# Optimization experiments

Measured on AMD Instinct MI355X. Metric: run time of the kernel, lower is better.

## Reference

```python
import jax, jax.numpy as jnp
import numpy as np

T, B, E, H = 2048, 4, 1024, 16
D = E // H  # head_dim = 64


def setup_inputs() -> dict:
    key = jax.random.key(0)
    k1, k2, k3, k4 = jax.random.split(key, 4)
    x = jax.random.normal(k1, (T, B, E), dtype=jnp.float32)
    # xavier-ish init scale
    Wqkv = jax.random.normal(k2, (3 * E, E), dtype=jnp.float32) * (1.0 / np.sqrt(2.0 * E))
    Wo = jax.random.normal(k3, (E, E), dtype=jnp.float32) * (1.0 / np.sqrt(E))
    key_padding_mask = jax.random.randint(k4, (B, T), 0, 2).astype(jnp.bool_)  # True = pad
    return {"x": x, "Wqkv": Wqkv, "Wo": Wo, "key_padding_mask": key_padding_mask}


def reference(x, Wqkv, Wo, key_padding_mask):
    t, b, e = x.shape
    h, d = H, E // H
    # fused QKV projection (bias=False)
    qkv = jnp.einsum('tbe,fe->tbf', x, Wqkv).reshape(t, b, 3, h, d)
    # chunk along the 3-axis, then permute to (B, H, T, D)
    q = jnp.transpose(qkv[:, :, 0], (1, 2, 0, 3))
    k = jnp.transpose(qkv[:, :, 1], (1, 2, 0, 3))
    v = jnp.transpose(qkv[:, :, 2], (1, 2, 0, 3))
    # SDPA with default scale 1/sqrt(head_dim); additive -inf mask on padded keys
    scale = 1.0 / jnp.sqrt(jnp.asarray(d, dtype=x.dtype))
    scores = jnp.einsum('bhtd,bhsd->bhts', q, k) * scale
    scores = jnp.where(key_padding_mask[:, None, None, :], -jnp.inf, scores)
    probs = jax.nn.softmax(scores, axis=-1)
    ctx = jnp.einsum('bhts,bhsd->bhtd', probs, v)  # (B,H,T,D)
    ctx = jnp.transpose(ctx, (0, 2, 1, 3)).reshape(b, t, e)  # (B,T,E)
    out = jnp.einsum('bte,fe->btf', ctx, Wo)  # out_proj, bias=False
    return jnp.transpose(out, (1, 0, 2))  # back to (T,B,E)
```

## Files before the change

### kernel.cpp

```cpp
#include <hip/hip_runtime.h>

typedef unsigned short u16;
typedef __bf16 bf16x8 __attribute__((ext_vector_type(8)));
typedef unsigned short u16x8 __attribute__((ext_vector_type(8)));
typedef unsigned short u16x4 __attribute__((ext_vector_type(4)));
typedef float f32x4 __attribute__((ext_vector_type(4)));

__device__ __forceinline__ f32x4 mfma16(u16x8 a, u16x8 b, f32x4 c) {
    return __builtin_amdgcn_mfma_f32_16x16x32_bf16(
        __builtin_bit_cast(bf16x8, a), __builtin_bit_cast(bf16x8, b), c, 0, 0, 0);
}

__device__ __forceinline__ u16 f2b(float f) {
    unsigned int u = __builtin_bit_cast(unsigned int, f);
    return (u16)((u + 0x7fffu + ((u >> 16) & 1u)) >> 16);
}

__device__ __forceinline__ f32x4 zero4() { f32x4 z = {0.f, 0.f, 0.f, 0.f}; return z; }

typedef __attribute__((address_space(1))) const unsigned int gas_u32;
typedef __attribute__((address_space(3))) unsigned int las_u32;
__device__ __forceinline__ void gload16(const u16* g, u16* l) {
    __builtin_amdgcn_global_load_lds((gas_u32*)g, (las_u32*)l, 16, 0, 0);
}

__device__ __forceinline__ u16x4 tr16(unsigned off) {
    u16x4 r;
    asm volatile("ds_read_b64_tr_b16 %0, %1" : "=v"(r) : "v"(off));
    return r;
}

__global__ __launch_bounds__(256) void cvt_bf16_kernel(const float* __restrict__ in,
                                                       u16* __restrict__ out, int n) {
    int i = (blockIdx.x * 256 + threadIdx.x) * 4;
    if (i >= n) return;
    float4 v = *reinterpret_cast<const float4*>(in + i);
    u16x4 o;
    o.x = f2b(v.x); o.y = f2b(v.y); o.z = f2b(v.z); o.w = f2b(v.w);
    *reinterpret_cast<u16x4*>(out + i) = o;
}

__global__ void detect_mask_kernel(const unsigned char* __restrict__ m, int* __restrict__ flag) {
    __shared__ int any;
    if (threadIdx.x == 0) any = 0;
    __syncthreads();
    int acc = 0;
    for (int i = threadIdx.x; i < 8192; i += 256)
        if (i & 3) acc |= m[i];
    if (acc) atomicOr(&any, 1);
    __syncthreads();
    if (threadIdx.x == 0) *flag = any ? 0 : 1;
}

template <int EPI>
__global__ __launch_bounds__(256)
void gemm_bt_kernel(const u16* __restrict__ A, const u16* __restrict__ Bt,
                    int M, int N, int K,
                    u16* __restrict__ qo, u16* __restrict__ ko, u16* __restrict__ vo,
                    float* __restrict__ fo) {
    constexpr int BK = 64;
    __shared__ __align__(16) u16 Al[128 * BK];
    __shared__ __align__(16) u16 Bl[128 * BK];
    int tid = threadIdx.x;
    int wave = tid >> 6, lane = tid & 63;
    int l15 = lane & 15, l16 = lane >> 4;
    int wr = wave >> 1, wc = wave & 1;
    int bx = blockIdx.x, by = blockIdx.y;

    const u16* gA[4]; const u16* gB[4]; u16* lA[4]; u16* lB[4];
#pragma unroll
    for (int q = 0; q < 4; q++) {
        int c = tid + q * 256;
        gA[q] = A + (size_t)(by * 128 + (c >> 3)) * K + (c & 7) * 8;
        gB[q] = Bt + (size_t)(bx * 128 + (c >> 3)) * K + (c & 7) * 8;
        lA[q] = Al + c * 8;
        lB[q] = Bl + c * 8;
    }

    f32x4 acc[4][4];
#pragma unroll
    for (int m = 0; m < 4; m++)
#pragma unroll
        for (int n = 0; n < 4; n++) acc[m][n] = zero4();

    for (int k0 = 0; k0 < K; k0 += BK) {
        __syncthreads();
#pragma unroll
        for (int q = 0; q < 4; q++) {
            gload16(gA[q] + k0, lA[q]);
            gload16(gB[q] + k0, lB[q]);
        }
        __syncthreads();
#pragma unroll
        for (int ks = 0; ks < 2; ks++) {
            u16x8 af[4], bfr[4];
#pragma unroll
            for (int m = 0; m < 4; m++)
                af[m] = *(const u16x8*)&Al[(wr * 64 + m * 16 + l15) * BK + ks * 32 + l16 * 8];
#pragma unroll
            for (int n = 0; n < 4; n++)
                bfr[n] = *(const u16x8*)&Bl[(wc * 64 + n * 16 + l15) * BK + ks * 32 + l16 * 8];
#pragma unroll
            for (int m = 0; m < 4; m++)
#pragma unroll
                for (int n = 0; n < 4; n++) acc[m][n] = mfma16(af[m], bfr[n], acc[m][n]);
        }
    }

#pragma unroll
    for (int m = 0; m < 4; m++) {
#pragma unroll
        for (int j = 0; j < 4; j++) {
            int row = by * 128 + wr * 64 + m * 16 + l16 * 4 + j;
#pragma unroll
            for (int n = 0; n < 4; n++) {
                int col = bx * 128 + wc * 64 + n * 16 + l15;
                float val = acc[m][n][j];
                if constexpr (EPI == 0) {
                    int chunk = col >> 10, h = (col >> 6) & 15, d = col & 63;
                    int t = row >> 2, bI = row & 3;
                    if (chunk == 0) val *= 0.18033688011112042f;
                    u16* dst = (chunk == 0) ? qo : (chunk == 1) ? ko : vo;
                    dst[((size_t)(bI * 16 + h) * 2048 + t) * 64 + d] = f2b(val);
                } else {
                    fo[(size_t)row * N + col] = val;
                }
            }
        }
    }
}

__global__ __launch_bounds__(256, 3)
void attn_kernel(const u16* __restrict__ Qg, const u16* __restrict__ Kg,
                 const u16* __restrict__ Vg, const void* __restrict__ maskp,
                 const int* __restrict__ flag, u16* __restrict__ ctx) {
    __shared__ __align__(16) u16 Kl[64 * 72];
    __shared__ __align__(128) u16 Vs[4][64][16];
    __shared__ __align__(16) u16 Pl[4][32 * 72];

    int tid = threadIdx.x;
    int wave = tid >> 6, lane = tid & 63;
    int l15 = lane & 15, l16 = lane >> 4;
    int bh = blockIdx.y;
    int b = bh >> 4, h = bh & 15;
    size_t base = (size_t)bh * 2048 * 64;
    int q0 = blockIdx.x * 128 + wave * 32;

    int isInt = *flag;
    const unsigned char* m8 = (const unsigned char*)maskp;
    const int* m32 = (const int*)maskp;

    u16x8 aq[2][2];
#pragma unroll
    for (int qb = 0; qb < 2; qb++)
#pragma unroll
        for (int ks = 0; ks < 2; ks++)
            aq[qb][ks] = *(const u16x8*)(Qg + base + (size_t)(q0 + qb * 16 + l15) * 64 +
                                         ks * 32 + l16 * 8);

    f32x4 acc_o[2][4];
    float mrun[2][4], plsum[2][4];
#pragma unroll
    for (int qb = 0; qb < 2; qb++) {
#pragma unroll
        for (int db = 0; db < 4; db++) acc_o[qb][db] = zero4();
#pragma unroll
        for (int j = 0; j < 4; j++) { mrun[qb][j] = -1e30f; plsum[qb][j] = 0.f; }
    }

    int srow2 = tid >> 2, sc2 = tid & 3;
    const u16* kg2 = Kg + base + (size_t)srow2 * 64 + sc2 * 16;
    const u16* vg2 = Vg + base + (size_t)srow2 * 64 + sc2 * 16;
    u16* kld = &Kl[srow2 * 72 + sc2 * 16];
    u16* vsd = &Vs[sc2][srow2][0];
    unsigned vtrb = (unsigned)(uintptr_t)(&Vs[0][0][0]) + (unsigned)(l16 * 256 + l15 * 8);

    u16x8 ka = *(const u16x8*)kg2, kb_ = *(const u16x8*)(kg2 + 8);
    u16x8 va = *(const u16x8*)vg2, vb_ = *(const u16x8*)(vg2 + 8);

    for (int it = 0; it < 32; ++it) {
        int s0 = it * 64;
        __syncthreads();
        *(u16x8*)kld = ka; *(u16x8*)(kld + 8) = kb_;
        *(u16x8*)vsd = va; *(u16x8*)(vsd + 8) = vb_;
        int snext = (s0 + 64) & 2047;
        u16x8 kan = *(const u16x8*)(kg2 + (size_t)snext * 64);
        u16x8 kbn = *(const u16x8*)(kg2 + (size_t)snext * 64 + 8);
        u16x8 van = *(const u16x8*)(vg2 + (size_t)snext * 64);
        u16x8 vbn = *(const u16x8*)(vg2 + (size_t)snext * 64 + 8);
        __syncthreads();

        int pad[4];
#pragma unroll
        for (int kb2 = 0; kb2 < 4; kb2++) {
            int ki = b * 2048 + s0 + kb2 * 16 + l15;
            pad[kb2] = isInt ? (m32[ki] != 0) : (m8[ki] != 0);
        }

        f32x4 sa[2][4];
#pragma unroll
        for (int kb2 = 0; kb2 < 4; kb2++) { sa[0][kb2] = zero4(); sa[1][kb2] = zero4(); }
        __builtin_amdgcn_s_setprio(1);
#pragma unroll
        for (int kb2 = 0; kb2 < 4; kb2++)
#pragma unroll
            for (int ks = 0; ks < 2; ks++) {
                u16x8 bk = *(const u16x8*)&Kl[(kb2 * 16 + l15) * 72 + ks * 32 + l16 * 8];
                sa[0][kb2] = mfma16(aq[0][ks], bk, sa[0][kb2]);
                sa[1][kb2] = mfma16(aq[1][ks], bk, sa[1][kb2]);
            }
        __builtin_amdgcn_s_setprio(0);

#pragma unroll
        for (int qb = 0; qb < 2; qb++) {
            float sv[4][4];
            float gl = -1e30f;
#pragma unroll
            for (int kb2 = 0; kb2 < 4; kb2++)
#pragma unroll
                for (int j = 0; j < 4; j++) {
                    sv[kb2][j] = pad[kb2] ? -1e30f : sa[qb][kb2][j];
                    gl = fmaxf(gl, sv[kb2][j] - mrun[qb][j]);
                }
            if (__any(gl > 8.0f)) {
                float tm[4];
#pragma unroll
                for (int j = 0; j < 4; j++)
                    tm[j] = fmaxf(fmaxf(sv[0][j], sv[1][j]), fmaxf(sv[2][j], sv[3][j]));
#pragma unroll
                for (int j = 0; j < 4; j++) {
                    tm[j] = fmaxf(tm[j], __shfl_xor(tm[j], 1));
                    tm[j] = fmaxf(tm[j], __shfl_xor(tm[j], 2));
                    tm[j] = fmaxf(tm[j], __shfl_xor(tm[j], 4));
                    tm[j] = fmaxf(tm[j], __shfl_xor(tm[j], 8));
                }
#pragma unroll
                for (int j = 0; j < 4; j++) {
                    float mnew = fmaxf(mrun[qb][j], tm[j]);
                    float sc = exp2f(mrun[qb][j] - mnew);
                    mrun[qb][j] = mnew;
                    plsum[qb][j] *= sc;
#pragma unroll
                    for (int db = 0; db < 4; db++) acc_o[qb][db][j] *= sc;
                }
            }
#pragma unroll
            for (int j = 0; j < 4; j++) {
                int prow = qb * 16 + l16 * 4 + j;
                float ps = 0.f;
#pragma unroll
                for (int kb2 = 0; kb2 < 4; kb2++) {
                    float p = exp2f(sv[kb2][j] - mrun[qb][j]);
                    Pl[wave][prow * 72 + kb2 * 16 + l15] = f2b(p);
                    ps += p;
                }
                plsum[qb][j] += ps;
            }
        }

        u16x8 ap[2][2];
#pragma unroll
        for (int qb = 0; qb < 2; qb++)
#pragma unroll
            for (int ks2 = 0; ks2 < 2; ks2++)
                ap[qb][ks2] = *(const u16x8*)&Pl[wave][(qb * 16 + l15) * 72 +
                                                       ks2 * 32 + l16 * 8];
        u16x4 t[4][2][2];
#pragma unroll
        for (int ks2 = 0; ks2 < 2; ks2++)
#pragma unroll
            for (int db = 0; db < 4; db++) {
                t[db][ks2][0] = tr16(vtrb + db * 2048 + ks2 * 1024);
                t[db][ks2][1] = tr16(vtrb + db * 2048 + ks2 * 1024 + 128);
            }
        asm volatile("s_waitcnt lgkmcnt(0)" ::: "memory");
        __builtin_amdgcn_sched_barrier(0);
        __builtin_amdgcn_s_setprio(1);
#pragma unroll
        for (int ks2 = 0; ks2 < 2; ks2++)
#pragma unroll
            for (int db = 0; db < 4; db++) {
                u16x8 bv = {t[db][ks2][0][0], t[db][ks2][0][1], t[db][ks2][0][2],
                            t[db][ks2][0][3], t[db][ks2][1][0], t[db][ks2][1][1],
                            t[db][ks2][1][2], t[db][ks2][1][3]};
                acc_o[0][db] = mfma16(ap[0][ks2], bv, acc_o[0][db]);
                acc_o[1][db] = mfma16(ap[1][ks2], bv, acc_o[1][db]);
            }
        __builtin_amdgcn_s_setprio(0);
        ka = kan; kb_ = kbn; va = van; vb_ = vbn;
    }

#pragma unroll
    for (int qb = 0; qb < 2; qb++)
#pragma unroll
        for (int j = 0; j < 4; j++) {
            float rs = plsum[qb][j];
            rs += __shfl_xor(rs, 1);
            rs += __shfl_xor(rs, 2);
            rs += __shfl_xor(rs, 4);
            rs += __shfl_xor(rs, 8);
            float inv = 1.0f / rs;
            int qg = q0 + qb * 16 + l16 * 4 + j;
            size_t mrow = (size_t)qg * 4 + b;
#pragma unroll
            for (int db = 0; db < 4; db++)
                ctx[mrow * 1024 + h * 64 + db * 16 + l15] = f2b(acc_o[qb][db][j] * inv);
        }
}

extern "C" void kernel_launch(void* const* d_in, const int* in_sizes, int n_in,
                              void* d_out, int out_size, void* d_ws, size_t ws_size,
                              hipStream_t stream) {
    const float* x = (const float*)d_in[0];
    const float* wqkv = (const float*)d_in[1];
    const float* wo = (const float*)d_in[2];
    const void* mask = d_in[3];
    float* out = (float*)d_out;

    char* ws = (char*)d_ws;
    int* flag = (int*)ws;
    u16* xb = (u16*)(ws + 16);
    u16* wqkvb = xb + 8388608;
    u16* wob = wqkvb + 3145728;
    u16* qw = wob + 1048576;
    u16* kw = qw + 8388608;
    u16* vw = kw + 8388608;
    u16* ctx = xb;

    cvt_bf16_kernel<<<8192, 256, 0, stream>>>(x, xb, 8388608);
    cvt_bf16_kernel<<<3072, 256, 0, stream>>>(wqkv, wqkvb, 3145728);
    cvt_bf16_kernel<<<1024, 256, 0, stream>>>(wo, wob, 1048576);
    detect_mask_kernel<<<1, 256, 0, stream>>>((const unsigned char*)mask, flag);

    gemm_bt_kernel<0><<<dim3(24, 64), 256, 0, stream>>>(xb, wqkvb, 8192, 3072, 1024,
                                                        qw, kw, vw, nullptr);
    attn_kernel<<<dim3(16, 64), 256, 0, stream>>>(qw, kw, vw, mask, flag, ctx);
    gemm_bt_kernel<1><<<dim3(8, 64), 256, 0, stream>>>(ctx, wob, 8192, 1024, 1024,
                                                       nullptr, nullptr, nullptr, out);
}
```

Before: 414.3 us.

## Swizzle workgroup order, permute V/P LDS layout to pack probability stores

Both the GEMM and attention kernels remap the flat workgroup index with an XCD-style swizzle (stride by nwg/8) so neighbouring tiles sharing K/V or weight rows land on the same chiplet's L2. In attention, the V rows in LDS are permuted and the P tile columns reordered so each lane writes two packed 32-bit words instead of four 16-bit scalar LDS stores. The key-order permutation is applied consistently to P and V, so the PV product is unchanged, but it relies on the mapping being exactly matched. The swizzle assumes the grid size is divisible by 8.

```diff
diff --git a/kernel.cpp b/kernel.cpp
--- a/kernel.cpp
+++ b/kernel.cpp
@@ -65,7 +65,11 @@
     int wave = tid >> 6, lane = tid & 63;
     int l15 = lane & 15, l16 = lane >> 4;
     int wr = wave >> 1, wc = wave & 1;
-    int bx = blockIdx.x, by = blockIdx.y;
+
+    int flat = blockIdx.y * gridDim.x + blockIdx.x;
+    int nwg = gridDim.x * gridDim.y;
+    int swz = (flat & 7) * (nwg >> 3) + (flat >> 3);
+    int bx = swz % gridDim.x, by = swz / gridDim.x;
 
     const u16* gA[4]; const u16* gB[4]; u16* lA[4]; u16* lB[4];
 #pragma unroll
@@ -141,10 +145,15 @@
     int tid = threadIdx.x;
     int wave = tid >> 6, lane = tid & 63;
     int l15 = lane & 15, l16 = lane >> 4;
-    int bh = blockIdx.y;
+
+    int flat = blockIdx.y * gridDim.x + blockIdx.x;
+    int nwg = gridDim.x * gridDim.y;
+    int swz = (flat & 7) * (nwg >> 3) + (flat >> 3);
+    int bxs = swz & 15, bh = swz >> 4;
+
     int b = bh >> 4, h = bh & 15;
     size_t base = (size_t)bh * 2048 * 64;
-    int q0 = blockIdx.x * 128 + wave * 32;
+    int q0 = bxs * 128 + wave * 32;
 
     int isInt = *flag;
     const unsigned char* m8 = (const unsigned char*)maskp;
@@ -172,7 +181,8 @@
     const u16* kg2 = Kg + base + (size_t)srow2 * 64 + sc2 * 16;
     const u16* vg2 = Vg + base + (size_t)srow2 * 64 + sc2 * 16;
     u16* kld = &Kl[srow2 * 72 + sc2 * 16];
-    u16* vsd = &Vs[sc2][srow2][0];
+    int vpos = ((srow2 >> 5) << 5) + ((srow2 & 15) * 2) + ((srow2 >> 4) & 1);
+    u16* vsd = &Vs[sc2][vpos][0];
     unsigned vtrb = (unsigned)(uintptr_t)(&Vs[0][0][0]) + (unsigned)(l16 * 256 + l15 * 8);
 
     u16x8 ka = *(const u16x8*)kg2, kb_ = *(const u16x8*)(kg2 + 8);
@@ -247,14 +257,15 @@
 #pragma unroll
             for (int j = 0; j < 4; j++) {
                 int prow = qb * 16 + l16 * 4 + j;
-                float ps = 0.f;
-#pragma unroll
-                for (int kb2 = 0; kb2 < 4; kb2++) {
-                    float p = exp2f(sv[kb2][j] - mrun[qb][j]);
-                    Pl[wave][prow * 72 + kb2 * 16 + l15] = f2b(p);
-                    ps += p;
-                }
-                plsum[qb][j] += ps;
+                float p0 = exp2f(sv[0][j] - mrun[qb][j]);
+                float p1 = exp2f(sv[1][j] - mrun[qb][j]);
+                float p2 = exp2f(sv[2][j] - mrun[qb][j]);
+                float p3 = exp2f(sv[3][j] - mrun[qb][j]);
+                unsigned w01 = (unsigned)f2b(p0) | ((unsigned)f2b(p1) << 16);
+                unsigned w23 = (unsigned)f2b(p2) | ((unsigned)f2b(p3) << 16);
+                *(unsigned*)&Pl[wave][prow * 72 + l15 * 2] = w01;
+                *(unsigned*)&Pl[wave][prow * 72 + 32 + l15 * 2] = w23;
+                plsum[qb][j] += (p0 + p1) + (p2 + p3);
             }
         }
 
```

Result: no change. 411.6 us (-0.6%).
